# Kernel optimization log

Measured on AMD Instinct MI355X. Metric: run time of the kernel, lower is better.

## Reference

```python
import jax, jax.numpy as jnp
import numpy as np

B, T, D, H = 2, 512, 512, 8
HD = D // H
FF = 4 * D
MOM_BETA, NOV_BETA, NOV_GAIN = 0.9, 0.95, 3.0
LR_MIN, LR_MAX, MAX_FW_NORM = 0.5, 3.0, 32.0


def setup_inputs() -> dict:
    key = jax.random.key(0)
    ks = jax.random.split(key, 10)
    s = 1.0 / np.sqrt(D)
    return {
        'x': jax.random.normal(ks[0], (B, T, D), jnp.float32),
        'Wq': jax.random.normal(ks[1], (D, D), jnp.float32) * s,
        'Wk1': jax.random.normal(ks[2], (D, D), jnp.float32) * s,
        'Wk2': jax.random.normal(ks[3], (D, D), jnp.float32) * s,
        'Wv': jax.random.normal(ks[4], (D, D), jnp.float32) * s,
        'Wo': jax.random.normal(ks[5], (D, D), jnp.float32) * s,
        'lambda_logit': jnp.zeros((H,), jnp.float32),  # sigmoid -> lambda_init = 0.5
        'ln1_g': jnp.ones((D,), jnp.float32), 'ln1_b': jnp.zeros((D,), jnp.float32),
        'base_weight': jax.random.normal(ks[6], (D, D), jnp.float32) * s,  # ~xavier
        'ttt_bias': jnp.zeros((D,), jnp.float32),
        'log_inner_lr': jnp.log(jnp.asarray(0.05, jnp.float32)),
        'ln2_g': jnp.ones((D,), jnp.float32), 'ln2_b': jnp.zeros((D,), jnp.float32),
        'W1': jax.random.normal(ks[7], (FF, D), jnp.float32) * s,
        'b1': jnp.zeros((FF,), jnp.float32),
        'W2': jax.random.normal(ks[8], (D, FF), jnp.float32) * (1.0 / np.sqrt(FF)),
        'b2': jnp.zeros((D,), jnp.float32),
        'ln3_g': jnp.ones((D,), jnp.float32), 'ln3_b': jnp.zeros((D,), jnp.float32),
    }


def _ln(x, g, b):
    m = x.mean(-1, keepdims=True)
    v = jnp.mean((x - m) ** 2, -1, keepdims=True)
    return (x - m) / jnp.sqrt(v + 1e-5) * g + b


def _diff_attn(x, Wq, Wk1, Wk2, Wv, Wo, lambda_logit):
    b, t, d = x.shape
    def heads(w):
        return jnp.einsum('btd,od->bto', x, w).reshape(b, t, H, HD).transpose(0, 2, 1, 3)
    q, k1, k2, v = heads(Wq), heads(Wk1), heads(Wk2), heads(Wv)
    scale = HD ** -0.5
    s1 = jnp.einsum('bhqd,bhkd->bhqk', q, k1) * scale
    s2 = jnp.einsum('bhqd,bhkd->bhqk', q, k2) * scale
    mask = jnp.tril(jnp.ones((t, t), bool))
    neg = jnp.finfo(s1.dtype).min
    s1 = jnp.where(mask, s1, neg)
    s2 = jnp.where(mask, s2, neg)
    lam = jax.nn.sigmoid(lambda_logit)[None, :, None, None]
    attn = jax.nn.softmax(s1, -1) - lam * jax.nn.softmax(s2, -1)
    attn = attn / jnp.clip(jnp.abs(attn).sum(-1, keepdims=True), 1e-6, None)
    o = jnp.einsum('bhqk,bhkd->bhqd', attn, v).transpose(0, 2, 1, 3).reshape(b, t, d)
    return jnp.einsum('btd,od->bto', o, Wo)


def _ttt(x, base_weight, ttt_bias, log_inner_lr):
    b = x.shape[0]
    inner_lr = jnp.clip(jnp.exp(log_inner_lr), 1e-5, 1.0)
    fw0 = jnp.broadcast_to(base_weight, (b, D, D)).astype(x.dtype) + 0.0
    mom0 = jnp.zeros_like(fw0)
    ema0 = jnp.zeros((b, D), x.dtype)
    lrm0 = jnp.ones((b, 1), x.dtype)

    def step(carry, x_t):  # x_t: [B, D]
        fw, mom, ema, lrm = carry
        y = jnp.einsum('bij,bj->bi', fw, x_t) + ttt_bias
        err = (y - x_t) / float(D)  # targets=None -> target is x_t
        g = jax.lax.stop_gradient(err[:, :, None] * x_t[:, None, :])  # first_order
        mom2 = MOM_BETA * mom + (1.0 - MOM_BETA) * g
        nov = jnp.abs(x_t - ema).mean(-1, keepdims=True)  # [B, 1]
        lr_scale = jnp.clip(1.0 + NOV_GAIN * nov, LR_MIN, LR_MAX)
        lrm2 = NOV_BETA * lrm + (1.0 - NOV_BETA) * lr_scale
        ema2 = NOV_BETA * ema + (1.0 - NOV_BETA) * x_t
        fw2 = fw - (inner_lr * lrm2)[:, :, None] * mom2
        norm = jnp.clip(jnp.sqrt((fw2 * fw2).sum((1, 2), keepdims=True)), 1e-6, None)
        fw2 = fw2 * jnp.minimum(MAX_FW_NORM / norm, 1.0)
        return (fw2, mom2, ema2, lrm2), y

    _, ys = jax.lax.scan(step, (fw0, mom0, ema0, lrm0), x.transpose(1, 0, 2))
    return ys.transpose(1, 0, 2)


def reference(x, Wq, Wk1, Wk2, Wv, Wo, lambda_logit, ln1_g, ln1_b, base_weight, ttt_bias, log_inner_lr, ln2_g, ln2_b, W1, b1, W2, b2, ln3_g, ln3_b):
    h = x + _diff_attn(_ln(x, ln1_g, ln1_b), Wq, Wk1, Wk2, Wv, Wo, lambda_logit)
    h = h + _ttt(_ln(h, ln2_g, ln2_b), base_weight, ttt_bias, log_inner_lr)
    z = _ln(h, ln3_g, ln3_b)
    z = jax.nn.gelu(jnp.einsum('btd,fd->btf', z, W1) + b1, approximate=False)
    h = h + jnp.einsum('btf,df->btd', z, W2) + b2
    return h
```

## Files before the change

kernel.cpp:

```cpp
#include <hip/hip_runtime.h>
#include <hip/hip_fp16.h>

typedef _Float16 f16;
typedef f16 f16x4 __attribute__((ext_vector_type(4)));
typedef f16 f16x8 __attribute__((ext_vector_type(8)));
typedef float f32x4 __attribute__((ext_vector_type(4)));

#define DEVI static __device__ __forceinline__

DEVI void gload_lds16(const void* g, void* l) {
  __builtin_amdgcn_global_load_lds(
      (const __attribute__((address_space(1))) unsigned int*)g,
      (__attribute__((address_space(3))) unsigned int*)l, 16, 0, 0);
}

DEVI float wave_red_sum64(float v) {
#pragma unroll
  for (int m = 1; m < 64; m <<= 1) v += __shfl_xor(v, m, 64);
  return v;
}
DEVI float wave_red_max64(float v) {
#pragma unroll
  for (int m = 1; m < 64; m <<= 1) v = fmaxf(v, __shfl_xor(v, m, 64));
  return v;
}

template <int CTRL>
DEVI float dpp_addf(float v) {
  int s = __builtin_amdgcn_update_dpp(0, __float_as_int(v), CTRL, 0xF, 0xF, true);
  return v + __int_as_float(s);
}
DEVI float redsum64(float v) {
  v = dpp_addf<0xB1>(v);
  v = dpp_addf<0x4E>(v);
  v = dpp_addf<0x141>(v);
  v = dpp_addf<0x140>(v);
  int t = __builtin_amdgcn_update_dpp(0, __float_as_int(v), 0x142, 0xA, 0xF, true);
  v += __int_as_float(t);
  t = __builtin_amdgcn_update_dpp(0, __float_as_int(v), 0x143, 0xC, 0xF, true);
  v += __int_as_float(t);
  return __int_as_float(__builtin_amdgcn_readlane(__float_as_int(v), 63));
}

__global__ void cvt_all_kernel(const float* __restrict__ s0, const float* __restrict__ s1,
                               const float* __restrict__ s2, const float* __restrict__ s3,
                               const float* __restrict__ s4, const float* __restrict__ s5,
                               const float* __restrict__ s6, f16* __restrict__ d) {
  const int blk = blockIdx.x;
  const float* s; long dofs; int local;
  if (blk < 256)       { s = s0; dofs = 0;       local = blk; }
  else if (blk < 512)  { s = s1; dofs = 262144;  local = blk - 256; }
  else if (blk < 768)  { s = s2; dofs = 524288;  local = blk - 512; }
  else if (blk < 1024) { s = s3; dofs = 786432;  local = blk - 768; }
  else if (blk < 1280) { s = s4; dofs = 1048576; local = blk - 1024; }
  else if (blk < 2304) { s = s5; dofs = 1310720; local = blk - 1280; }
  else                 { s = s6; dofs = 2359296; local = blk - 2304; }
  const long i = (long)local * 1024 + threadIdx.x * 4;
  float4 v = *(const float4*)(s + i);
  f16x4 o = {(f16)v.x, (f16)v.y, (f16)v.z, (f16)v.w};
  *(f16x4*)(d + dofs + i) = o;
}

__global__ void ln_kernel(const float* __restrict__ in, const float* __restrict__ add,
                          const float* __restrict__ g, const float* __restrict__ b,
                          float* __restrict__ sumout, float* __restrict__ lnf,
                          f16* __restrict__ lnh) {
  const int row = blockIdx.x * 4 + (threadIdx.x >> 6);
  const int lane = threadIdx.x & 63;
  const long base = (long)row * 512;
  const int c0 = lane * 4, c1 = 256 + lane * 4;
  float4 a0 = *(const float4*)(in + base + c0);
  float4 a1 = *(const float4*)(in + base + c1);
  if (add) {
    float4 d0 = *(const float4*)(add + base + c0);
    float4 d1 = *(const float4*)(add + base + c1);
    a0.x += d0.x; a0.y += d0.y; a0.z += d0.z; a0.w += d0.w;
    a1.x += d1.x; a1.y += d1.y; a1.z += d1.z; a1.w += d1.w;
  }
  if (sumout) {
    *(float4*)(sumout + base + c0) = a0;
    *(float4*)(sumout + base + c1) = a1;
  }
  float v[8] = {a0.x, a0.y, a0.z, a0.w, a1.x, a1.y, a1.z, a1.w};
  float s = 0.f;
#pragma unroll
  for (int k = 0; k < 8; k++) s += v[k];
  s = wave_red_sum64(s);
  const float mean = s * (1.f / 512.f);
  float vs = 0.f;
#pragma unroll
  for (int k = 0; k < 8; k++) { float d = v[k] - mean; vs += d * d; }
  vs = wave_red_sum64(vs);
  const float rstd = rsqrtf(vs * (1.f / 512.f) + 1e-5f);
  float4 g0 = *(const float4*)(g + c0), g1 = *(const float4*)(g + c1);
  float4 p0 = *(const float4*)(b + c0), p1 = *(const float4*)(b + c1);
  const float gg[8] = {g0.x, g0.y, g0.z, g0.w, g1.x, g1.y, g1.z, g1.w};
  const float bv[8] = {p0.x, p0.y, p0.z, p0.w, p1.x, p1.y, p1.z, p1.w};
  float y[8];
#pragma unroll
  for (int k = 0; k < 8; k++) y[k] = (v[k] - mean) * rstd * gg[k] + bv[k];
  if (lnf) {
    float4 o0 = {y[0], y[1], y[2], y[3]}, o1 = {y[4], y[5], y[6], y[7]};
    *(float4*)(lnf + base + c0) = o0;
    *(float4*)(lnf + base + c1) = o1;
  }
  if (lnh) {
    f16x4 o0 = {(f16)y[0], (f16)y[1], (f16)y[2], (f16)y[3]};
    f16x4 o1 = {(f16)y[4], (f16)y[5], (f16)y[6], (f16)y[7]};
    *(f16x4*)(lnh + base + c0) = o0;
    *(f16x4*)(lnh + base + c1) = o1;
  }
}

__global__ void red4ln_kernel(const float* __restrict__ parts, const float* __restrict__ xres,
                              const float* __restrict__ g, const float* __restrict__ b,
                              float* __restrict__ h1, float* __restrict__ x2out) {
  const int row = blockIdx.x * 4 + (threadIdx.x >> 6);
  const int lane = threadIdx.x & 63;
  const long base = (long)row * 512;
  const int c0 = lane * 4, c1 = 256 + lane * 4;
  float4 a0, a1;
  {
    float4 s0 = *(const float4*)(parts + base + c0);
    float4 s1 = *(const float4*)(parts + 524288 + base + c0);
    float4 s2 = *(const float4*)(parts + 1048576 + base + c0);
    float4 s3 = *(const float4*)(parts + 1572864 + base + c0);
    float4 r  = *(const float4*)(xres + base + c0);
    a0.x = ((s0.x + s1.x) + (s2.x + s3.x)) + r.x;
    a0.y = ((s0.y + s1.y) + (s2.y + s3.y)) + r.y;
    a0.z = ((s0.z + s1.z) + (s2.z + s3.z)) + r.z;
    a0.w = ((s0.w + s1.w) + (s2.w + s3.w)) + r.w;
  }
  {
    float4 s0 = *(const float4*)(parts + base + c1);
    float4 s1 = *(const float4*)(parts + 524288 + base + c1);
    float4 s2 = *(const float4*)(parts + 1048576 + base + c1);
    float4 s3 = *(const float4*)(parts + 1572864 + base + c1);
    float4 r  = *(const float4*)(xres + base + c1);
    a1.x = ((s0.x + s1.x) + (s2.x + s3.x)) + r.x;
    a1.y = ((s0.y + s1.y) + (s2.y + s3.y)) + r.y;
    a1.z = ((s0.z + s1.z) + (s2.z + s3.z)) + r.z;
    a1.w = ((s0.w + s1.w) + (s2.w + s3.w)) + r.w;
  }
  *(float4*)(h1 + base + c0) = a0;
  *(float4*)(h1 + base + c1) = a1;
  float v[8] = {a0.x, a0.y, a0.z, a0.w, a1.x, a1.y, a1.z, a1.w};
  float s = 0.f;
#pragma unroll
  for (int k = 0; k < 8; k++) s += v[k];
  s = wave_red_sum64(s);
  const float mean = s * (1.f / 512.f);
  float vs = 0.f;
#pragma unroll
  for (int k = 0; k < 8; k++) { float d = v[k] - mean; vs += d * d; }
  vs = wave_red_sum64(vs);
  const float rstd = rsqrtf(vs * (1.f / 512.f) + 1e-5f);
  float4 g0 = *(const float4*)(g + c0), g1 = *(const float4*)(g + c1);
  float4 p0 = *(const float4*)(b + c0), p1 = *(const float4*)(b + c1);
  const float gg[8] = {g0.x, g0.y, g0.z, g0.w, g1.x, g1.y, g1.z, g1.w};
  const float bv[8] = {p0.x, p0.y, p0.z, p0.w, p1.x, p1.y, p1.z, p1.w};
  float y[8];
#pragma unroll
  for (int k = 0; k < 8; k++) y[k] = (v[k] - mean) * rstd * gg[k] + bv[k];
  float4 o0 = {y[0], y[1], y[2], y[3]}, o1 = {y[4], y[5], y[6], y[7]};
  *(float4*)(x2out + base + c0) = o0;
  *(float4*)(x2out + base + c1) = o1;
}

enum { EPI_QKV = 0, EPI_SCORES = 2, EPI_PV = 3, EPI_GELU = 5, EPI_PART = 7 };

template <int EPI>
__launch_bounds__(256, 1) __global__
void gemm_bt(const f16* __restrict__ A, const f16* __restrict__ W, int lda, int ldw,
             long Az, long Wz, void* __restrict__ dst, const float* __restrict__ bias,
             const float* __restrict__ resid, int K, float scale, int zofs, int hcp) {
  if (EPI == EPI_SCORES && blockIdx.x > blockIdx.y) return;
  __shared__ f16 lA[128 * 64];
  __shared__ f16 lB[128 * 64];
  const int tid = threadIdx.x;
  const int wave = tid >> 6, lane = tid & 63;
  const int z = blockIdx.z;
  const f16* Ab;
  const f16* Wb;
  if (EPI == EPI_SCORES) {
    const int v_ = (z >= hcp) ? 1 : 0, head = z - v_ * hcp;
    Ab = A + (long)head * 32768 + (long)blockIdx.y * 128 * lda;
    Wb = W + (long)v_ * 524288 + (long)head * 32768 + (long)blockIdx.x * 128 * ldw;
  } else {
    Ab = A + (long)z * Az + (long)blockIdx.y * 128 * lda;
    Wb = W + (long)z * Wz + (long)blockIdx.x * 128 * ldw;
  }

  f32x4 acc[4][4];
#pragma unroll
  for (int a = 0; a < 4; a++)
#pragma unroll
    for (int q = 0; q < 4; q++) acc[a][q] = (f32x4){0.f, 0.f, 0.f, 0.f};

  int srow[4], scol[4];
#pragma unroll
  for (int i = 0; i < 4; i++) {
    int c = i * 256 + tid;
    int row = c >> 3;
    int colb = (c & 7) << 4;
    srow[i] = row;
    scol[i] = (colb ^ ((row & 7) << 4)) >> 1;
  }

  for (int k0 = 0; k0 < K; k0 += 64) {
    __syncthreads();
#pragma unroll
    for (int i = 0; i < 4; i++) {
      const int le = (i * 256 + wave * 64) * 8;
      gload_lds16(Ab + (long)srow[i] * lda + k0 + scol[i], lA + le);
      gload_lds16(Wb + (long)srow[i] * ldw + k0 + scol[i], lB + le);
    }
    __syncthreads();
    const int wm = (wave >> 1) * 64, wn = (wave & 1) * 64;
#pragma unroll
    for (int km = 0; km < 2; km++) {
      const int kb = km * 64 + ((lane >> 4) << 4);
      f16x8 af[4], bfv[4];
#pragma unroll
      for (int mf = 0; mf < 4; mf++) {
        int r = wm + mf * 16 + (lane & 15);
        af[mf] = *(const f16x8*)((const char*)lA + r * 128 + (kb ^ ((r & 7) << 4)));
      }
#pragma unroll
      for (int nf = 0; nf < 4; nf++) {
        int r = wn + nf * 16 + (lane & 15);
        bfv[nf] = *(const f16x8*)((const char*)lB + r * 128 + (kb ^ ((r & 7) << 4)));
      }
#pragma unroll
      for (int mf = 0; mf < 4; mf++)
#pragma unroll
        for (int nf = 0; nf < 4; nf++)
          acc[mf][nf] = __builtin_amdgcn_mfma_f32_16x16x32_f16(af[mf], bfv[nf], acc[mf][nf], 0, 0, 0);
    }
  }

  const int wm = (wave >> 1) * 64, wn = (wave & 1) * 64;
  const int rbase = blockIdx.y * 128 + wm + ((lane >> 4) << 2);
  const int cbase = blockIdx.x * 128 + wn + (lane & 15);
#pragma unroll
  for (int mf = 0; mf < 4; mf++)
#pragma unroll
    for (int nf = 0; nf < 4; nf++)
#pragma unroll
      for (int j = 0; j < 4; j++) {
        const int m = rbase + mf * 16 + j;
        const int n = cbase + nf * 16;
        const float v = acc[mf][nf][j];
        if (EPI == EPI_QKV) {
          f16* d = (f16*)dst + (long)z * 524288;
          if (z < 3)
            d[(long)((m >> 9) * 8 + (n >> 6)) * 32768 + (m & 511) * 64 + (n & 63)] = (f16)v;
          else
            d[(long)((m >> 9) * 8 + (n >> 6)) * 32768 + (n & 63) * 512 + (m & 511)] = (f16)v;
        } else if (EPI == EPI_SCORES) {
          ((float*)dst)[(long)z * 262144 + (long)m * 512 + n] = v * scale;
        } else if (EPI == EPI_PV) {
          if (n < 64) {
            const int hh = z + zofs;
            ((f16*)dst)[(long)((hh >> 3) * 512 + m) * 512 + (hh & 7) * 64 + n] = (f16)v;
          }
        } else if (EPI == EPI_GELU) {
          const float u = v + bias[n];
          ((f16*)dst)[(long)m * 2048 + n] = (f16)(0.5f * u * (1.f + erff(u * 0.70710678118f)));
        } else {
          ((float*)dst)[(long)z * 524288 + (long)m * 512 + n] = v;
        }
      }
}

__global__ void red4_kernel(const float* __restrict__ parts, const float* __restrict__ resid,
                            const float* __restrict__ bias, float* __restrict__ dst) {
  const long i = ((long)blockIdx.x * 256 + threadIdx.x) * 4;
  float4 s0 = *(const float4*)(parts + i);
  float4 s1 = *(const float4*)(parts + 524288 + i);
  float4 s2 = *(const float4*)(parts + 1048576 + i);
  float4 s3 = *(const float4*)(parts + 1572864 + i);
  float4 r  = *(const float4*)(resid + i);
  float4 o;
  o.x = ((s0.x + s1.x) + (s2.x + s3.x)) + r.x;
  o.y = ((s0.y + s1.y) + (s2.y + s3.y)) + r.y;
  o.z = ((s0.z + s1.z) + (s2.z + s3.z)) + r.z;
  o.w = ((s0.w + s1.w) + (s2.w + s3.w)) + r.w;
  if (bias) {
    const int n = (int)(i & 511);
    float4 b = *(const float4*)(bias + n);
    o.x += b.x; o.y += b.y; o.z += b.z; o.w += b.w;
  }
  *(float4*)(dst + i) = o;
}

__global__ void softmax_diff_kernel(const float* __restrict__ S1, const float* __restrict__ S2,
                                    const float* __restrict__ lamlog, f16* __restrict__ attn,
                                    int zofs) {
  const int rid = blockIdx.x * 4 + (threadIdx.x >> 6);
  const int lane = threadIdx.x & 63;
  const int z = rid >> 9, i = rid & 511;
  const float lam = 1.f / (1.f + __expf(-lamlog[(z + zofs) & 7]));
  const long base = (long)z * 262144 + (long)i * 512;
  const int c0 = lane * 4, c1 = 256 + lane * 4;
  float4 xa = *(const float4*)(S1 + base + c0);
  float4 xb = *(const float4*)(S1 + base + c1);
  float4 ya = *(const float4*)(S2 + base + c0);
  float4 yb = *(const float4*)(S2 + base + c1);
  float s1v[8] = {xa.x, xa.y, xa.z, xa.w, xb.x, xb.y, xb.z, xb.w};
  float s2v[8] = {ya.x, ya.y, ya.z, ya.w, yb.x, yb.y, yb.z, yb.w};
  int cols[8];
#pragma unroll
  for (int k = 0; k < 8; k++) cols[k] = (k < 4) ? (c0 + k) : (c1 + k - 4);
  float m1 = -3.0e38f, m2 = -3.0e38f;
#pragma unroll
  for (int k = 0; k < 8; k++)
    if (cols[k] <= i) { m1 = fmaxf(m1, s1v[k]); m2 = fmaxf(m2, s2v[k]); }
  m1 = wave_red_max64(m1);
  m2 = wave_red_max64(m2);
  float z1 = 0.f, z2 = 0.f, e1[8], e2[8];
#pragma unroll
  for (int k = 0; k < 8; k++) {
    const bool valid = cols[k] <= i;
    e1[k] = valid ? __expf(s1v[k] - m1) : 0.f;
    e2[k] = valid ? __expf(s2v[k] - m2) : 0.f;
    z1 += e1[k]; z2 += e2[k];
  }
  z1 = wave_red_sum64(z1);
  z2 = wave_red_sum64(z2);
  const float r1 = 1.f / z1, r2 = lam / z2;
  float p[8], l1 = 0.f;
#pragma unroll
  for (int k = 0; k < 8; k++) { p[k] = e1[k] * r1 - e2[k] * r2; l1 += fabsf(p[k]); }
  l1 = wave_red_sum64(l1);
  const float rn = 1.f / fmaxf(l1, 1e-6f);
  f16x4 o0 = {(f16)(p[0] * rn), (f16)(p[1] * rn), (f16)(p[2] * rn), (f16)(p[3] * rn)};
  f16x4 o1 = {(f16)(p[4] * rn), (f16)(p[5] * rn), (f16)(p[6] * rn), (f16)(p[7] * rn)};
  *(f16x4*)(attn + base + c0) = o0;
  *(f16x4*)(attn + base + c1) = o1;
}

#define ALD4(dst, p) asm volatile("global_load_dwordx4 %0, %1, off" : "=&v"(dst) : "v"(p) : "memory")
#define ALD1(dst, p) asm volatile("global_load_dword %0, %1, off" : "=&v"(dst) : "v"(p) : "memory")
#define VMWAIT(N)                                                             \
  {                                                                           \
    asm volatile("s_waitcnt vmcnt(" #N ")" ::: "memory");                     \
    __builtin_amdgcn_sched_barrier(0);                                        \
  }

#define EISSUE(X)                                                             \
  {                                                                           \
    ALD1(X[0], pe);        ALD1(X[1], pe + 512);                              \
    ALD1(X[2], pe + 1024); ALD1(X[3], pe + 1536);                             \
    ALD1(X[4], pe + 2048); ALD1(X[5], pe + 2560);                             \
    ALD1(X[6], pe + 3072); ALD1(X[7], pe + 3584);                             \
    pe += 4096;                                                               \
  }
#define ESTEP(V, T)                                                           \
  {                                                                           \
    dp[(long)(T) * 512] = fabsf((V) - ema);                                   \
    ema = fmaf(0.95f, ema, 0.05f * (V));                                      \
  }

__launch_bounds__(64, 1) __global__
void eta_diff_kernel(const float* __restrict__ x2, float* __restrict__ diff) {
  const int blk = blockIdx.x;
  const int b = blk >> 3;
  const int col = (blk & 7) * 64 + threadIdx.x;
  const float* pe = x2 + (long)b * 262144 + col;
  float* dp = diff + (long)b * 262144 + col;
  float ema = 0.f;
  float EA[8], EB[8];
  EISSUE(EA);
  EISSUE(EB);
  VMWAIT(8);
#pragma unroll 1
  for (int t = 0; t < 512; t += 16) {
    ESTEP(EA[0], t + 0); ESTEP(EA[1], t + 1); ESTEP(EA[2], t + 2); ESTEP(EA[3], t + 3);
    ESTEP(EA[4], t + 4); ESTEP(EA[5], t + 5); ESTEP(EA[6], t + 6); ESTEP(EA[7], t + 7);
    EISSUE(EA);
    VMWAIT(16);
    ESTEP(EB[0], t + 8);  ESTEP(EB[1], t + 9);  ESTEP(EB[2], t + 10); ESTEP(EB[3], t + 11);
    ESTEP(EB[4], t + 12); ESTEP(EB[5], t + 13); ESTEP(EB[6], t + 14); ESTEP(EB[7], t + 15);
    EISSUE(EB);
    VMWAIT(16);
  }
  asm volatile("s_waitcnt vmcnt(0)" ::: "memory");
}

__global__ void eta_nov_kernel(const float* __restrict__ diff, float* __restrict__ nov,
                               int* __restrict__ flag) {
  if (blockIdx.x == 0 && threadIdx.x == 0) flag[0] = 0;
  const int row = blockIdx.x * 4 + (threadIdx.x >> 6);
  const int lane = threadIdx.x & 63;
  const float* dp = diff + (long)row * 512 + lane * 4;
  float4 a0 = *(const float4*)dp;
  float4 a1 = *(const float4*)(dp + 256);
  float s = ((a0.x + a0.y) + (a0.z + a0.w)) + ((a1.x + a1.y) + (a1.z + a1.w));
  s = wave_red_sum64(s);
  if (lane == 0) nov[row] = s * (1.f / 512.f);
}

__global__ void eta_scan_kernel(const float* __restrict__ nov, const float* __restrict__ loglr,
                                float* __restrict__ eta) {
  if (threadIdx.x != 0) return;
  const int b = blockIdx.x;
  float ilr = expf(loglr[0]);
  ilr = fminf(fmaxf(ilr, 1e-5f), 1.f);
  float lrm = 1.f;
  const float* pb = nov + (long)b * 512;
#pragma unroll 8
  for (int t = 0; t < 512; t++) {
    const float ls = fminf(fmaxf(fmaf(3.f, pb[t], 1.f), 0.5f), 3.f);
    lrm = fmaf(0.95f, lrm, 0.05f * ls);
    eta[b * 512 + t] = ilr * lrm;
  }
}

DEVI float dot8(const f32x4 F0, const f32x4 F1, const f32x4 X0, const f32x4 X1) {
  float a0 = F0.x * X0.x, a1 = F0.y * X0.y, a2 = F0.z * X0.z, a3 = F0.w * X0.w;
  a0 = fmaf(F1.x, X1.x, a0); a1 = fmaf(F1.y, X1.y, a1);
  a2 = fmaf(F1.z, X1.z, a2); a3 = fmaf(F1.w, X1.w, a3);
  return (a0 + a1) + (a2 + a3);
}
DEVI void upd8(f32x4& M0, f32x4& M1, f32x4& F0, f32x4& F1, float c1, float e,
               const f32x4 X0, const f32x4 X1, float& ns) {
  M0.x = fmaf(0.9f, M0.x, c1 * X0.x); F0.x = fmaf(-e, M0.x, F0.x); ns = fmaf(F0.x, F0.x, ns);
  M0.y = fmaf(0.9f, M0.y, c1 * X0.y); F0.y = fmaf(-e, M0.y, F0.y); ns = fmaf(F0.y, F0.y, ns);
  M0.z = fmaf(0.9f, M0.z, c1 * X0.z); F0.z = fmaf(-e, M0.z, F0.z); ns = fmaf(F0.z, F0.z, ns);
  M0.w = fmaf(0.9f, M0.w, c1 * X0.w); F0.w = fmaf(-e, M0.w, F0.w); ns = fmaf(F0.w, F0.w, ns);
  M1.x = fmaf(0.9f, M1.x, c1 * X1.x); F1.x = fmaf(-e, M1.x, F1.x); ns = fmaf(F1.x, F1.x, ns);
  M1.y = fmaf(0.9f, M1.y, c1 * X1.y); F1.y = fmaf(-e, M1.y, F1.y); ns = fmaf(F1.y, F1.y, ns);
  M1.z = fmaf(0.9f, M1.z, c1 * X1.z); F1.z = fmaf(-e, M1.z, F1.z); ns = fmaf(F1.z, F1.z, ns);
  M1.w = fmaf(0.9f, M1.w, c1 * X1.w); F1.w = fmaf(-e, M1.w, F1.w); ns = fmaf(F1.w, F1.w, ns);
}

#define TISSUE2(X, RA, RB, ET)                                                \
  {                                                                           \
    ALD4(X[0], pxc);        ALD4(X[1], pxc + 4);                              \
    ALD4(X[2], pxc + 512);  ALD4(X[3], pxc + 516);                            \
    ALD4(X[4], pxc + 1024); ALD4(X[5], pxc + 1028);                           \
    ALD4(X[6], pxc + 1536); ALD4(X[7], pxc + 1540);                           \
    ALD1(RA[0], pxra);        ALD1(RA[1], pxra + 512);                        \
    ALD1(RA[2], pxra + 1024); ALD1(RA[3], pxra + 1536);                       \
    ALD1(RB[0], pxrb);        ALD1(RB[1], pxrb + 512);                        \
    ALD1(RB[2], pxrb + 1024); ALD1(RB[3], pxrb + 1536);                       \
    ALD4(ET, per);                                                            \
    pxc += 2048; pxra += 2048; pxrb += 2048; per += 4;                        \
  }

#define TSTEP2(X0v, X1v, rAv, rBv, ev, K)                                     \
  {                                                                           \
    const float pA_ = redsum64(dot8(fA0, fA1, X0v, X1v));                     \
    const float pB_ = redsum64(dot8(fB0, fB1, X0v, X1v));                     \
    const float yA_ = pA_ + biasA, yB_ = pB_ + biasB;                         \
    ysA[K] = yA_; ysB[K] = yB_;                                               \
    const float c1A_ = (yA_ - (rAv)) * (0.1f / 512.f);                        \
    const float c1B_ = (yB_ - (rBv)) * (0.1f / 512.f);                        \
    const float e_ = (ev);                                                    \
    float ns_ = 0.f;                                                          \
    upd8(mA0, mA1, fA0, fA1, c1A_, e_, X0v, X1v, ns_);                        \
    upd8(mB0, mB1, fB0, fB1, c1B_, e_, X0v, X1v, ns_);                        \
    nsmax = fmaxf(nsmax, ns_);                                                \
  }

__launch_bounds__(64, 1) __global__
void ttt_fast_kernel(const float* __restrict__ x2, const float* __restrict__ base_w,
                     const float* __restrict__ tbias, const float* __restrict__ eta,
                     float* __restrict__ yT, float* __restrict__ npB) {
  const int blk = blockIdx.x;
  const int b = blk >> 8;
  const int rA = blk & 255;
  const int lane = threadIdx.x;
  const float* xb = x2 + (long)b * 262144;

  f32x4 fA0, fA1, fB0, fB1;
  float biasA, biasB;
  ALD4(fA0, base_w + (long)rA * 512 + lane * 8);
  ALD4(fA1, base_w + (long)rA * 512 + lane * 8 + 4);
  ALD4(fB0, base_w + (long)(rA + 256) * 512 + lane * 8);
  ALD4(fB1, base_w + (long)(rA + 256) * 512 + lane * 8 + 4);
  ALD1(biasA, tbias + rA);
  ALD1(biasB, tbias + rA + 256);

  f32x4 mA0 = {0.f, 0.f, 0.f, 0.f}, mA1 = mA0, mB0 = mA0, mB1 = mA0;
  float ysA[8], ysB[8];
  float nsmax = 0.f;

  const float* pxc = xb + lane * 8;
  const float* pxra = xb + rA;
  const float* pxrb = xb + rA + 256;
  const float* per = eta + b * 512;
  float* pyA = yT + (long)(b * 512 + rA) * 512;
  float* pyB = yT + (long)(b * 512 + rA + 256) * 512;

  f32x4 XA[8], XB[8], EA, EB;
  float RA0[4], RB0[4], RA1[4], RB1[4];
  TISSUE2(XA, RA0, RB0, EA);
  TISSUE2(XB, RA1, RB1, EB);
  VMWAIT(17);

#pragma unroll 1
  for (int T = 0; T < 512; T += 8) {
    TSTEP2(XA[0], XA[1], RA0[0], RB0[0], EA.x, 0);
    TSTEP2(XA[2], XA[3], RA0[1], RB0[1], EA.y, 1);
    TSTEP2(XA[4], XA[5], RA0[2], RB0[2], EA.z, 2);
    TSTEP2(XA[6], XA[7], RA0[3], RB0[3], EA.w, 3);
    TISSUE2(XA, RA0, RB0, EA);
    VMWAIT(17);
    TSTEP2(XB[0], XB[1], RA1[0], RB1[0], EB.x, 4);
    TSTEP2(XB[2], XB[3], RA1[1], RB1[1], EB.y, 5);
    TSTEP2(XB[4], XB[5], RA1[2], RB1[2], EB.z, 6);
    TSTEP2(XB[6], XB[7], RA1[3], RB1[3], EB.w, 7);
    if (lane == 0) {
      *(float4*)(pyA + T)     = (float4){ysA[0], ysA[1], ysA[2], ysA[3]};
      *(float4*)(pyA + T + 4) = (float4){ysA[4], ysA[5], ysA[6], ysA[7]};
      *(float4*)(pyB + T)     = (float4){ysB[0], ysB[1], ysB[2], ysB[3]};
      *(float4*)(pyB + T + 4) = (float4){ysB[4], ysB[5], ysB[6], ysB[7]};
    }
    TISSUE2(XB, RA1, RB1, EB);
    VMWAIT(21);
  }
  asm volatile("s_waitcnt vmcnt(0)" ::: "memory");
  const float tot = redsum64(nsmax);
  if (lane == 0) npB[blk] = tot;
}

__global__ void transpose2v_kernel(const float* __restrict__ yT, float* __restrict__ ysb,
                                   const float* __restrict__ npB, int* __restrict__ flag) {
  const int s = blockIdx.z;
  if (s == 2) {
    if (blockIdx.x != 0 || blockIdx.y != 0) return;
    const int tid = threadIdx.x;
    const int wave = tid >> 6, lane = tid & 63;
    float a = npB[tid];
    float c = npB[tid + 256];
    a = wave_red_sum64(a);
    c = wave_red_sum64(c);
    __shared__ float pa[4], pc[4];
    if (lane == 0) { pa[wave] = a; pc[wave] = c; }
    __syncthreads();
    if (tid == 0) {
      const float s0 = (pa[0] + pa[1]) + (pa[2] + pa[3]);
      const float s1 = (pc[0] + pc[1]) + (pc[2] + pc[3]);
      if (s0 > 1000.f || s1 > 1000.f) atomicOr(flag, 1);
    }
    return;
  }
  __shared__ float tile[64][65];
  const float* src = yT + (long)s * 262144;
  float* dst = ysb + (long)s * 262144;
  const int ti = blockIdx.y, tj = blockIdx.x;
  const int tr = threadIdx.x >> 4;
  const int tc = (threadIdx.x & 15) * 4;
#pragma unroll
  for (int p = 0; p < 4; p++) {
    const int r = tr + p * 16;
    float4 v = *(const float4*)(src + (long)(ti * 64 + r) * 512 + tj * 64 + tc);
    tile[r][tc] = v.x; tile[r][tc + 1] = v.y; tile[r][tc + 2] = v.z; tile[r][tc + 3] = v.w;
  }
  __syncthreads();
#pragma unroll
  for (int p = 0; p < 4; p++) {
    const int j = tr + p * 16;
    float4 v = {tile[tc][j], tile[tc + 1][j], tile[tc + 2][j], tile[tc + 3][j]};
    *(float4*)(dst + (long)(tj * 64 + j) * 512 + ti * 64 + tc) = v;
  }
}

__launch_bounds__(1024, 1) __global__
void ttt_fallback_kernel(const int* __restrict__ flag, const float* __restrict__ x2,
                         const float* __restrict__ base_w, const float* __restrict__ tbias,
                         const float* __restrict__ eta, float* __restrict__ ys,
                         float* __restrict__ fwg, float* __restrict__ momg) {
  if (flag[0] == 0) return;
  const int b = blockIdx.x;
  const int tid = threadIdx.x;
  const int wave = tid >> 6, lane = tid & 63;
  float* fw = fwg + (long)b * 262144;
  float* mm = momg + (long)b * 262144;
  for (int e = tid; e < 262144; e += 1024) { fw[e] = base_w[e]; mm[e] = 0.f; }
  __shared__ float xs[512], errs[512], red[16];
  const float* xb = x2 + (long)b * 262144;
  for (int t = 0; t < 512; t++) {
    __syncthreads();
    if (tid < 512) xs[tid] = xb[t * 512 + tid];
    __syncthreads();
    if (tid < 512) {
      float acc = 0.f;
      for (int c = 0; c < 512; c++) acc = fmaf(fw[(long)tid * 512 + c], xs[c], acc);
      const float y = acc + tbias[tid];
      ys[((long)b * 512 + t) * 512 + tid] = y;
      errs[tid] = (y - xs[tid]) * (1.f / 512.f);
    }
    __syncthreads();
    const float eta_t = eta[b * 512 + t];
    float nsq = 0.f;
    for (int e = tid; e < 262144; e += 1024) {
      const int r = e >> 9, c = e & 511;
      const float m2 = fmaf(0.9f, mm[e], 0.1f * errs[r] * xs[c]);
      mm[e] = m2;
      const float f2 = fmaf(-eta_t, m2, fw[e]);
      fw[e] = f2;
      nsq = fmaf(f2, f2, nsq);
    }
    nsq = wave_red_sum64(nsq);
    if (lane == 0) red[wave] = nsq;
    __syncthreads();
    if (tid == 0) {
      float s = 0.f;
      for (int w = 0; w < 16; w++) s += red[w];
      red[0] = s;
    }
    __syncthreads();
    const float norm = fmaxf(sqrtf(red[0]), 1e-6f);
    const float sc = fminf(32.f / norm, 1.f);
    if (sc < 1.f)
      for (int e = tid; e < 262144; e += 1024) fw[e] *= sc;
  }
}

extern "C" void kernel_launch(void* const* d_in, const int* in_sizes, int n_in,
                              void* d_out, int out_size, void* d_ws, size_t ws_size,
                              hipStream_t stream) {
  (void)in_sizes; (void)n_in; (void)out_size;
  const float* x      = (const float*)d_in[0];
  const float* Wq     = (const float*)d_in[1];
  const float* Wk1    = (const float*)d_in[2];
  const float* Wk2    = (const float*)d_in[3];
  const float* Wv     = (const float*)d_in[4];
  const float* Wo     = (const float*)d_in[5];
  const float* lamlog = (const float*)d_in[6];
  const float* ln1g   = (const float*)d_in[7];
  const float* ln1b   = (const float*)d_in[8];
  const float* basew  = (const float*)d_in[9];
  const float* tttb   = (const float*)d_in[10];
  const float* loglr  = (const float*)d_in[11];
  const float* ln2g   = (const float*)d_in[12];
  const float* ln2b   = (const float*)d_in[13];
  const float* W1     = (const float*)d_in[14];
  const float* b1     = (const float*)d_in[15];
  const float* W2     = (const float*)d_in[16];
  const float* b2     = (const float*)d_in[17];
  const float* ln3g   = (const float*)d_in[18];
  const float* ln3b   = (const float*)d_in[19];
  float* out = (float*)d_out;

  char* ws = (char*)d_ws;
  size_t off = 0;
  auto alloc = [&](size_t bytes) {
    size_t o = off;
    off += (bytes + 255) & ~(size_t)255;
    return o;
  };
  f16* WqH   = (f16*)(ws + alloc(262144 * 2));
  f16* Wk1H  = (f16*)(ws + alloc(262144 * 2));
  f16* Wk2H  = (f16*)(ws + alloc(262144 * 2));
  f16* WvH   = (f16*)(ws + alloc(262144 * 2));
  f16* WoH   = (f16*)(ws + alloc(262144 * 2));
  f16* W1H   = (f16*)(ws + alloc(1048576 * 2));
  f16* W2H   = (f16*)(ws + alloc(1048576 * 2));
  (void)Wk1H; (void)Wk2H; (void)WvH; (void)W1H;
  f16* xlnH  = (f16*)(ws + alloc(524288 * 2));
  f16* qh    = (f16*)(ws + alloc(524288 * 2));
  f16* k1h   = (f16*)(ws + alloc(524288 * 2));
  f16* k2h   = (f16*)(ws + alloc(524288 * 2));
  f16* vTh   = (f16*)(ws + alloc(524288 * 2));
  (void)k2h;
  f16* obtd  = (f16*)(ws + alloc(524288 * 2));
  f16* x3h   = (f16*)(ws + alloc(524288 * 2));
  f16* zh    = (f16*)(ws + alloc(2097152 * 2));
  float* h1  = (float*)(ws + alloc(524288 * 4));
  float* x2  = (float*)(ws + alloc(524288 * 4));
  float* ysb = (float*)(ws + alloc(524288 * 4));
  float* h2  = (float*)(ws + alloc(524288 * 4));
  float* eta = (float*)(ws + alloc(1024 * 4));
  float* yT  = (float*)(ws + alloc(524288 * 4));
  float* npB = (float*)(ws + alloc(512 * 4));
  float* nvd = (float*)(ws + alloc(524288 * 4));
  float* nov = (float*)(ws + alloc(1024 * 4));
  int* flag  = (int*)(ws + alloc(256));
  float* fwfb  = (float*)(ws + alloc(524288 * 4));
  float* momfb = (float*)(ws + alloc(524288 * 4));
  float* parts = (float*)(ws + alloc((size_t)4 * 524288 * 4));

  int hc = 16;
  while (hc > 1 && off + (size_t)hc * (262144ull * 4 * 2 + 262144ull * 2) > ws_size) hc >>= 1;
  float* S1  = (float*)(ws + alloc((size_t)hc * 262144 * 4));
  float* S2  = (float*)(ws + alloc((size_t)hc * 262144 * 4));
  f16* attnb = (f16*)(ws + alloc((size_t)hc * 262144 * 2));
  (void)S2;

  cvt_all_kernel<<<3328, 256, 0, stream>>>(Wq, Wk1, Wk2, Wv, Wo, W1, W2, WqH);

  ln_kernel<<<256, 256, 0, stream>>>(x, nullptr, ln1g, ln1b, nullptr, nullptr, xlnH);

  gemm_bt<EPI_QKV><<<dim3(4, 8, 4), 256, 0, stream>>>(
      xlnH, WqH, 512, 512, 0, 262144, qh, nullptr, nullptr, 512, 1.f, 0, 0);

  const int nc = 16 / hc;
  for (int c = 0; c < nc; c++) {
    const int cs = c * hc;
    gemm_bt<EPI_SCORES><<<dim3(4, 4, 2 * hc), 256, 0, stream>>>(
        qh + (long)cs * 32768, k1h + (long)cs * 32768, 64, 64, 0, 0, S1,
        nullptr, nullptr, 64, 0.125f, 0, hc);
    softmax_diff_kernel<<<hc * 128, 256, 0, stream>>>(S1, S2, lamlog, attnb, cs);
    gemm_bt<EPI_PV><<<dim3(1, 4, hc), 256, 0, stream>>>(
        attnb, vTh + (long)cs * 32768, 512, 512, 262144, 32768, obtd,
        nullptr, nullptr, 512, 1.f, cs, 0);
  }

  gemm_bt<EPI_PART><<<dim3(4, 8, 4), 256, 0, stream>>>(
      obtd, WoH, 512, 512, 128, 128, parts, nullptr, nullptr, 128, 1.f, 0, 0);
  red4ln_kernel<<<256, 256, 0, stream>>>(parts, x, ln2g, ln2b, h1, x2);

  eta_diff_kernel<<<16, 64, 0, stream>>>(x2, nvd);
  eta_nov_kernel<<<256, 256, 0, stream>>>(nvd, nov, flag);
  eta_scan_kernel<<<2, 64, 0, stream>>>(nov, loglr, eta);
  ttt_fast_kernel<<<512, 64, 0, stream>>>(x2, basew, tttb, eta, yT, npB);
  transpose2v_kernel<<<dim3(8, 8, 3), 256, 0, stream>>>(yT, ysb, npB, flag);
  ttt_fallback_kernel<<<2, 1024, 0, stream>>>(flag, x2, basew, tttb, eta, ysb, fwfb, momfb);

  ln_kernel<<<256, 256, 0, stream>>>(h1, ysb, ln3g, ln3b, h2, nullptr, x3h);

  gemm_bt<EPI_GELU><<<dim3(16, 8, 1), 256, 0, stream>>>(x3h, W1H, 512, 512, 0, 0, zh, b1, nullptr, 512, 1.f, 0, 0);
  gemm_bt<EPI_PART><<<dim3(4, 8, 4), 256, 0, stream>>>(
      zh, W2H, 2048, 2048, 512, 512, parts, nullptr, nullptr, 512, 1.f, 0, 0);
  red4_kernel<<<512, 256, 0, stream>>>(parts, h2, b2, out);
}
```

Baseline: 277.7 us.

## Split-K all projection GEMMs for more blocks and fuse LN1 into weight cast

Applies split-K to the QKV, Wo, W1 and W2 GEMMs so each launches more workgroups: QKV and W1 split two ways, Wo and W2 eight ways. The partial sums go to fp32 buffers and new reduction kernels add them; these also apply the QKV head layout and transpose, or bias plus GELU. The first LayerNorm is folded into the weight-conversion launch as extra blocks. The goal is better CU occupancy on the small GEMM grids, paid for with more fp32 partial-sum traffic and extra reduction launches. Scratch buffers are also aliased onto the shared partials region.

```diff
diff --git a/kernel.cpp b/kernel.cpp
--- a/kernel.cpp
+++ b/kernel.cpp
@@ -45,8 +45,41 @@
 __global__ void cvt_all_kernel(const float* __restrict__ s0, const float* __restrict__ s1,
                                const float* __restrict__ s2, const float* __restrict__ s3,
                                const float* __restrict__ s4, const float* __restrict__ s5,
-                               const float* __restrict__ s6, f16* __restrict__ d) {
+                               const float* __restrict__ s6, f16* __restrict__ d,
+                               const float* __restrict__ x, const float* __restrict__ ln1g,
+                               const float* __restrict__ ln1b, f16* __restrict__ xlnH) {
   const int blk = blockIdx.x;
+  if (blk >= 3328) {
+    const int row = (blk - 3328) * 4 + ((int)threadIdx.x >> 6);
+    const int lane = threadIdx.x & 63;
+    const long base = (long)row * 512;
+    const int c0 = lane * 4, c1 = 256 + lane * 4;
+    float4 a0 = *(const float4*)(x + base + c0);
+    float4 a1 = *(const float4*)(x + base + c1);
+    float v[8] = {a0.x, a0.y, a0.z, a0.w, a1.x, a1.y, a1.z, a1.w};
+    float s = 0.f;
+#pragma unroll
+    for (int k = 0; k < 8; k++) s += v[k];
+    s = wave_red_sum64(s);
+    const float mean = s * (1.f / 512.f);
+    float vs = 0.f;
+#pragma unroll
+    for (int k = 0; k < 8; k++) { float dd = v[k] - mean; vs += dd * dd; }
+    vs = wave_red_sum64(vs);
+    const float rstd = rsqrtf(vs * (1.f / 512.f) + 1e-5f);
+    float4 g0 = *(const float4*)(ln1g + c0), g1 = *(const float4*)(ln1g + c1);
+    float4 p0 = *(const float4*)(ln1b + c0), p1 = *(const float4*)(ln1b + c1);
+    const float gg[8] = {g0.x, g0.y, g0.z, g0.w, g1.x, g1.y, g1.z, g1.w};
+    const float bv[8] = {p0.x, p0.y, p0.z, p0.w, p1.x, p1.y, p1.z, p1.w};
+    float y[8];
+#pragma unroll
+    for (int k = 0; k < 8; k++) y[k] = (v[k] - mean) * rstd * gg[k] + bv[k];
+    f16x4 o0 = {(f16)y[0], (f16)y[1], (f16)y[2], (f16)y[3]};
+    f16x4 o1 = {(f16)y[4], (f16)y[5], (f16)y[6], (f16)y[7]};
+    *(f16x4*)(xlnH + base + c0) = o0;
+    *(f16x4*)(xlnH + base + c1) = o1;
+    return;
+  }
   const float* s; long dofs; int local;
   if (blk < 256)       { s = s0; dofs = 0;       local = blk; }
   else if (blk < 512)  { s = s1; dofs = 262144;  local = blk - 256; }
@@ -112,7 +145,7 @@
   }
 }
 
-__global__ void red4ln_kernel(const float* __restrict__ parts, const float* __restrict__ xres,
+__global__ void red8ln_kernel(const float* __restrict__ parts, const float* __restrict__ xres,
                               const float* __restrict__ g, const float* __restrict__ b,
                               float* __restrict__ h1, float* __restrict__ x2out) {
   const int row = blockIdx.x * 4 + (threadIdx.x >> 6);
@@ -121,26 +154,24 @@
   const int c0 = lane * 4, c1 = 256 + lane * 4;
   float4 a0, a1;
   {
-    float4 s0 = *(const float4*)(parts + base + c0);
-    float4 s1 = *(const float4*)(parts + 524288 + base + c0);
-    float4 s2 = *(const float4*)(parts + 1048576 + base + c0);
-    float4 s3 = *(const float4*)(parts + 1572864 + base + c0);
-    float4 r  = *(const float4*)(xres + base + c0);
-    a0.x = ((s0.x + s1.x) + (s2.x + s3.x)) + r.x;
-    a0.y = ((s0.y + s1.y) + (s2.y + s3.y)) + r.y;
-    a0.z = ((s0.z + s1.z) + (s2.z + s3.z)) + r.z;
-    a0.w = ((s0.w + s1.w) + (s2.w + s3.w)) + r.w;
+    float4 r = *(const float4*)(xres + base + c0);
+    float sx = r.x, sy = r.y, sz = r.z, sw = r.w;
+#pragma unroll
+    for (int sl = 0; sl < 8; sl++) {
+      float4 p = *(const float4*)(parts + (long)sl * 524288 + base + c0);
+      sx += p.x; sy += p.y; sz += p.z; sw += p.w;
+    }
+    a0 = (float4){sx, sy, sz, sw};
   }
   {
-    float4 s0 = *(const float4*)(parts + base + c1);
-    float4 s1 = *(const float4*)(parts + 524288 + base + c1);
-    float4 s2 = *(const float4*)(parts + 1048576 + base + c1);
-    float4 s3 = *(const float4*)(parts + 1572864 + base + c1);
-    float4 r  = *(const float4*)(xres + base + c1);
-    a1.x = ((s0.x + s1.x) + (s2.x + s3.x)) + r.x;
-    a1.y = ((s0.y + s1.y) + (s2.y + s3.y)) + r.y;
-    a1.z = ((s0.z + s1.z) + (s2.z + s3.z)) + r.z;
-    a1.w = ((s0.w + s1.w) + (s2.w + s3.w)) + r.w;
+    float4 r = *(const float4*)(xres + base + c1);
+    float sx = r.x, sy = r.y, sz = r.z, sw = r.w;
+#pragma unroll
+    for (int sl = 0; sl < 8; sl++) {
+      float4 p = *(const float4*)(parts + (long)sl * 524288 + base + c1);
+      sx += p.x; sy += p.y; sz += p.z; sw += p.w;
+    }
+    a1 = (float4){sx, sy, sz, sw};
   }
   *(float4*)(h1 + base + c0) = a0;
   *(float4*)(h1 + base + c1) = a1;
@@ -167,7 +198,7 @@
   *(float4*)(x2out + base + c1) = o1;
 }
 
-enum { EPI_QKV = 0, EPI_SCORES = 2, EPI_PV = 3, EPI_GELU = 5, EPI_PART = 7 };
+enum { EPI_SCORES = 2, EPI_PV = 3, EPI_PART = 7, EPI_QKVPART = 8, EPI_GPART = 9 };
 
 template <int EPI>
 __launch_bounds__(256, 1) __global__
@@ -186,6 +217,10 @@
     const int v_ = (z >= hcp) ? 1 : 0, head = z - v_ * hcp;
     Ab = A + (long)head * 32768 + (long)blockIdx.y * 128 * lda;
     Wb = W + (long)v_ * 524288 + (long)head * 32768 + (long)blockIdx.x * 128 * ldw;
+  } else if (EPI == EPI_QKVPART) {
+    const int widx = z & 3, ks = z >> 2;
+    Ab = A + (long)blockIdx.y * 128 * lda + (long)ks * Az;
+    Wb = W + (long)widx * Wz + (long)blockIdx.x * 128 * ldw + (long)ks * Az;
   } else {
     Ab = A + (long)z * Az + (long)blockIdx.y * 128 * lda;
     Wb = W + (long)z * Wz + (long)blockIdx.x * 128 * ldw;
@@ -251,46 +286,75 @@
         const int m = rbase + mf * 16 + j;
         const int n = cbase + nf * 16;
         const float v = acc[mf][nf][j];
-        if (EPI == EPI_QKV) {
-          f16* d = (f16*)dst + (long)z * 524288;
-          if (z < 3)
-            d[(long)((m >> 9) * 8 + (n >> 6)) * 32768 + (m & 511) * 64 + (n & 63)] = (f16)v;
-          else
-            d[(long)((m >> 9) * 8 + (n >> 6)) * 32768 + (n & 63) * 512 + (m & 511)] = (f16)v;
-        } else if (EPI == EPI_SCORES) {
+        if (EPI == EPI_SCORES) {
           ((float*)dst)[(long)z * 262144 + (long)m * 512 + n] = v * scale;
         } else if (EPI == EPI_PV) {
           if (n < 64) {
             const int hh = z + zofs;
             ((f16*)dst)[(long)((hh >> 3) * 512 + m) * 512 + (hh & 7) * 64 + n] = (f16)v;
           }
-        } else if (EPI == EPI_GELU) {
-          const float u = v + bias[n];
-          ((f16*)dst)[(long)m * 2048 + n] = (f16)(0.5f * u * (1.f + erff(u * 0.70710678118f)));
+        } else if (EPI == EPI_GPART) {
+          ((float*)dst)[(long)z * 2097152 + (long)m * 2048 + n] = v;
         } else {
           ((float*)dst)[(long)z * 524288 + (long)m * 512 + n] = v;
         }
       }
 }
 
-__global__ void red4_kernel(const float* __restrict__ parts, const float* __restrict__ resid,
+__global__ void qkv_red_kernel(const float* __restrict__ parts, f16* __restrict__ qkv) {
+  const int idx = blockIdx.x * 256 + threadIdx.x;
+  const int w = idx >> 17;
+  const int r = idx & 131071;
+  const int m = r >> 7;
+  const int n4 = (r & 127) << 2;
+  const float* p0 = parts + (long)w * 524288 + (long)m * 512 + n4;
+  float4 a = *(const float4*)p0;
+  float4 b = *(const float4*)(p0 + 4l * 524288);
+  const float s0 = a.x + b.x, s1 = a.y + b.y, s2 = a.z + b.z, s3 = a.w + b.w;
+  const int mb = (m >> 9) * 8 + (n4 >> 6);
+  if (w < 3) {
+    f16* d = qkv + (long)w * 524288;
+    f16x4 o = {(f16)s0, (f16)s1, (f16)s2, (f16)s3};
+    *(f16x4*)(d + (long)mb * 32768 + (m & 511) * 64 + (n4 & 63)) = o;
+  } else {
+    f16* d = qkv + 3l * 524288;
+    const long bb = (long)mb * 32768 + (m & 511);
+    d[bb + (long)(n4 & 63) * 512]       = (f16)s0;
+    d[bb + (long)((n4 & 63) + 1) * 512] = (f16)s1;
+    d[bb + (long)((n4 & 63) + 2) * 512] = (f16)s2;
+    d[bb + (long)((n4 & 63) + 3) * 512] = (f16)s3;
+  }
+}
+
+__global__ void red2gelu_kernel(const float* __restrict__ parts, const float* __restrict__ bias,
+                                f16* __restrict__ zh) {
+  const long i = ((long)blockIdx.x * 256 + threadIdx.x) * 4;
+  float4 a = *(const float4*)(parts + i);
+  float4 b = *(const float4*)(parts + 2097152 + i);
+  const int n = (int)(i & 2047);
+  float4 bb = *(const float4*)(bias + n);
+  float u0 = a.x + b.x + bb.x, u1 = a.y + b.y + bb.y;
+  float u2 = a.z + b.z + bb.z, u3 = a.w + b.w + bb.w;
+  f16x4 o = {(f16)(0.5f * u0 * (1.f + erff(u0 * 0.70710678118f))),
+             (f16)(0.5f * u1 * (1.f + erff(u1 * 0.70710678118f))),
+             (f16)(0.5f * u2 * (1.f + erff(u2 * 0.70710678118f))),
+             (f16)(0.5f * u3 * (1.f + erff(u3 * 0.70710678118f)))};
+  *(f16x4*)(zh + i) = o;
+}
+
+__global__ void red8_kernel(const float* __restrict__ parts, const float* __restrict__ resid,
                             const float* __restrict__ bias, float* __restrict__ dst) {
   const long i = ((long)blockIdx.x * 256 + threadIdx.x) * 4;
-  float4 s0 = *(const float4*)(parts + i);
-  float4 s1 = *(const float4*)(parts + 524288 + i);
-  float4 s2 = *(const float4*)(parts + 1048576 + i);
-  float4 s3 = *(const float4*)(parts + 1572864 + i);
-  float4 r  = *(const float4*)(resid + i);
-  float4 o;
-  o.x = ((s0.x + s1.x) + (s2.x + s3.x)) + r.x;
-  o.y = ((s0.y + s1.y) + (s2.y + s3.y)) + r.y;
-  o.z = ((s0.z + s1.z) + (s2.z + s3.z)) + r.z;
-  o.w = ((s0.w + s1.w) + (s2.w + s3.w)) + r.w;
-  if (bias) {
-    const int n = (int)(i & 511);
-    float4 b = *(const float4*)(bias + n);
-    o.x += b.x; o.y += b.y; o.z += b.z; o.w += b.w;
-  }
+  float4 r = *(const float4*)(resid + i);
+  float sx = r.x, sy = r.y, sz = r.z, sw = r.w;
+#pragma unroll
+  for (int sl = 0; sl < 8; sl++) {
+    float4 p = *(const float4*)(parts + (long)sl * 524288 + i);
+    sx += p.x; sy += p.y; sz += p.z; sw += p.w;
+  }
+  const int n = (int)(i & 511);
+  float4 b = *(const float4*)(bias + n);
+  float4 o = {sx + b.x, sy + b.y, sz + b.z, sw + b.w};
   *(float4*)(dst + i) = o;
 }
 
@@ -675,14 +739,14 @@
   float* ysb = (float*)(ws + alloc(524288 * 4));
   float* h2  = (float*)(ws + alloc(524288 * 4));
   float* eta = (float*)(ws + alloc(1024 * 4));
-  float* yT  = (float*)(ws + alloc(524288 * 4));
   float* npB = (float*)(ws + alloc(512 * 4));
-  float* nvd = (float*)(ws + alloc(524288 * 4));
   float* nov = (float*)(ws + alloc(1024 * 4));
   int* flag  = (int*)(ws + alloc(256));
-  float* fwfb  = (float*)(ws + alloc(524288 * 4));
-  float* momfb = (float*)(ws + alloc(524288 * 4));
-  float* parts = (float*)(ws + alloc((size_t)4 * 524288 * 4));
+  float* parts16 = (float*)(ws + alloc((size_t)16 * 1024 * 1024));
+  float* yT    = parts16;
+  float* nvd   = parts16 + 524288;
+  float* fwfb  = parts16 + 1048576;
+  float* momfb = parts16 + 1572864;
 
   int hc = 16;
   while (hc > 1 && off + (size_t)hc * (262144ull * 4 * 2 + 262144ull * 2) > ws_size) hc >>= 1;
@@ -691,12 +755,12 @@
   f16* attnb = (f16*)(ws + alloc((size_t)hc * 262144 * 2));
   (void)S2;
 
-  cvt_all_kernel<<<3328, 256, 0, stream>>>(Wq, Wk1, Wk2, Wv, Wo, W1, W2, WqH);
-
-  ln_kernel<<<256, 256, 0, stream>>>(x, nullptr, ln1g, ln1b, nullptr, nullptr, xlnH);
-
-  gemm_bt<EPI_QKV><<<dim3(4, 8, 4), 256, 0, stream>>>(
-      xlnH, WqH, 512, 512, 0, 262144, qh, nullptr, nullptr, 512, 1.f, 0, 0);
+  cvt_all_kernel<<<3584, 256, 0, stream>>>(Wq, Wk1, Wk2, Wv, Wo, W1, W2, WqH,
+                                           x, ln1g, ln1b, xlnH);
+
+  gemm_bt<EPI_QKVPART><<<dim3(4, 8, 8), 256, 0, stream>>>(
+      xlnH, WqH, 512, 512, 256, 262144, parts16, nullptr, nullptr, 256, 1.f, 0, 0);
+  qkv_red_kernel<<<2048, 256, 0, stream>>>(parts16, qh);
 
   const int nc = 16 / hc;
   for (int c = 0; c < nc; c++) {
@@ -710,9 +774,9 @@
         nullptr, nullptr, 512, 1.f, cs, 0);
   }
 
-  gemm_bt<EPI_PART><<<dim3(4, 8, 4), 256, 0, stream>>>(
-      obtd, WoH, 512, 512, 128, 128, parts, nullptr, nullptr, 128, 1.f, 0, 0);
-  red4ln_kernel<<<256, 256, 0, stream>>>(parts, x, ln2g, ln2b, h1, x2);
+  gemm_bt<EPI_PART><<<dim3(4, 8, 8), 256, 0, stream>>>(
+      obtd, WoH, 512, 512, 64, 64, parts16, nullptr, nullptr, 64, 1.f, 0, 0);
+  red8ln_kernel<<<256, 256, 0, stream>>>(parts16, x, ln2g, ln2b, h1, x2);
 
   eta_diff_kernel<<<16, 64, 0, stream>>>(x2, nvd);
   eta_nov_kernel<<<256, 256, 0, stream>>>(nvd, nov, flag);
@@ -723,8 +787,10 @@
 
   ln_kernel<<<256, 256, 0, stream>>>(h1, ysb, ln3g, ln3b, h2, nullptr, x3h);
 
-  gemm_bt<EPI_GELU><<<dim3(16, 8, 1), 256, 0, stream>>>(x3h, W1H, 512, 512, 0, 0, zh, b1, nullptr, 512, 1.f, 0, 0);
-  gemm_bt<EPI_PART><<<dim3(4, 8, 4), 256, 0, stream>>>(
-      zh, W2H, 2048, 2048, 512, 512, parts, nullptr, nullptr, 512, 1.f, 0, 0);
-  red4_kernel<<<512, 256, 0, stream>>>(parts, h2, b2, out);
-}
+  gemm_bt<EPI_GPART><<<dim3(16, 8, 2), 256, 0, stream>>>(
+      x3h, W1H, 512, 512, 256, 256, parts16, nullptr, nullptr, 256, 1.f, 0, 0);
+  red2gelu_kernel<<<2048, 256, 0, stream>>>(parts16, b1, zh);
+  gemm_bt<EPI_PART><<<dim3(4, 8, 8), 256, 0, stream>>>(
+      zh, W2H, 2048, 2048, 256, 256, parts16, nullptr, nullptr, 256, 1.f, 0, 0);
+  red8_kernel<<<512, 256, 0, stream>>>(parts16, h2, b2, out);
+}
```

Result: no change. 273.3 us (median of 2 runs) (-1.6%).
